# Performance work log

Hardware: AMD Instinct MI355X
Metric: run time of the kernel (lower is better)

The kernel has to match this reference:

```python
import jax, jax.numpy as jnp
import numpy as np

N_NODES = 100000
N_EDGES = 1600000
NUM_RELS = 200
NUM_BASES = 4
IN_FEAT = 20   # hardcoded by `view(-1, 1, 20)` in the torch source
OUT_FEAT = 20
SUBMAT_IN = IN_FEAT // NUM_BASES   # 5
SUBMAT_OUT = OUT_FEAT // NUM_BASES # 5


def setup_inputs() -> dict:
    key = jax.random.key(0)
    ks = jax.random.split(key, 9)
    return {
        "h": jax.random.normal(ks[0], (N_NODES, IN_FEAT), dtype=jnp.float32),
        "weight": jax.random.normal(ks[1], (NUM_RELS, NUM_BASES * SUBMAT_IN * SUBMAT_OUT), dtype=jnp.float32),
        "bias_term": jax.random.normal(ks[2], (NUM_RELS, OUT_FEAT), dtype=jnp.float32),
        "gate_weight": jax.random.normal(ks[3], (NUM_RELS, OUT_FEAT, 1), dtype=jnp.float32),
        "gate_bias": jax.random.normal(ks[4], (NUM_RELS, 1), dtype=jnp.float32),
        "loop_weight": jax.random.normal(ks[5], (IN_FEAT, OUT_FEAT), dtype=jnp.float32),
        "edge_src": jax.random.randint(ks[6], (N_EDGES,), 0, N_NODES, dtype=jnp.int32),
        "edge_dst": jax.random.randint(ks[7], (N_EDGES,), 0, N_NODES, dtype=jnp.int32),
        "etype": jax.random.randint(ks[8], (NUM_RELS,), 0, NUM_RELS, dtype=jnp.int32) if False else jax.random.randint(ks[8], (N_EDGES,), 0, NUM_RELS, dtype=jnp.int32),
    }


def reference(h, weight, bias_term, gate_weight, gate_bias, loop_weight, edge_src, edge_dst, etype):
    n_nodes = h.shape[0]
    # self-loop message (dropout=0.0 -> identity)
    loop_message = h @ loop_weight                                    # [N, out]
    # per-edge relation-indexed gathers
    W = weight[etype].reshape(-1, NUM_BASES, SUBMAT_IN, SUBMAT_OUT)   # [E, B, si, so]
    src = h[edge_src]                                                 # [E, in]
    node = src.reshape(-1, NUM_BASES, SUBMAT_IN)                      # [E, B, si]
    # block-diagonal small matmul
    msg = jnp.einsum('ebi,ebio->ebo', node, W).reshape(-1, OUT_FEAT)  # [E, out]
    # gate: sigmoid(<full src node, gate_weight_r> + gate_bias_r)
    gw = gate_weight[etype, :, 0]                                     # [E, out(=20=in)]
    gb = gate_bias[etype, 0]                                          # [E]
    gate = jax.nn.sigmoid(jnp.sum(src * gw, axis=-1) + gb)            # [E]
    msg = gate[:, None] * (msg + bias_term[etype])                    # [E, out]
    # scatter-sum aggregation to destination nodes (zero init for isolated nodes)
    agg = jax.ops.segment_sum(msg, edge_dst, num_segments=n_nodes)    # [N, out]
    return jax.nn.relu(agg + loop_message)
```

## Files before the change

kernel.cpp:

```cpp
#include <hip/hip_runtime.h>
#include <hip/hip_fp16.h>
#include <math.h>

#define IN_FEAT 20
#define OUT_FEAT 20
#define NUM_BASES 4
#define SUBMAT_IN 5
#define SUBMAT_OUT 5
#define NUM_RELS 200
#define CAP 64
#define NPB 160
#define BCAP 3072
#define EPB 4096


__global__ void __launch_bounds__(256)
hpad_zero_kernel(const float* __restrict__ h, __half* __restrict__ h_pad,
                 int* __restrict__ cursor, int n_nodes, int nb) {
    int v = blockIdx.x * 256 + threadIdx.x;
    if (v < nb) cursor[v] = 0;
    if (v >= n_nodes) return;
    const float4* hp = (const float4*)(h + (size_t)v * IN_FEAT);
    float4 a = hp[0], b = hp[1], c = hp[2], d = hp[3], e = hp[4];
    __half2 p0 = __floats2half2_rn(a.x, a.y), p1 = __floats2half2_rn(a.z, a.w);
    __half2 p2 = __floats2half2_rn(b.x, b.y), p3 = __floats2half2_rn(b.z, b.w);
    __half2 p4 = __floats2half2_rn(c.x, c.y), p5 = __floats2half2_rn(c.z, c.w);
    __half2 p6 = __floats2half2_rn(d.x, d.y), p7 = __floats2half2_rn(d.z, d.w);
    __half2 p8 = __floats2half2_rn(e.x, e.y), p9 = __floats2half2_rn(e.z, e.w);
    uint4 w0, w1; uint2 w2;
    w0.x = *(unsigned*)&p0; w0.y = *(unsigned*)&p1; w0.z = *(unsigned*)&p2; w0.w = *(unsigned*)&p3;
    w1.x = *(unsigned*)&p4; w1.y = *(unsigned*)&p5; w1.z = *(unsigned*)&p6; w1.w = *(unsigned*)&p7;
    w2.x = *(unsigned*)&p8; w2.y = *(unsigned*)&p9;
    char* dst = (char*)(h_pad + (size_t)v * 32);
    *(uint4*)(dst)      = w0;
    *(uint4*)(dst + 16) = w1;
    *(uint2*)(dst + 32) = w2;
}

__global__ void __launch_bounds__(1024)
bucket_scatter_kernel(const int* __restrict__ edge_src,
                      const int* __restrict__ edge_dst,
                      const int* __restrict__ etype,
                      int* __restrict__ cursor,
                      int2* __restrict__ bucketed,
                      int n_edges, int nb) {
    __shared__ int  lhist[640];
    __shared__ int  lofs[640];
    __shared__ int  lrank[640];
    __shared__ int  lbase[640];
    __shared__ int2 img[EPB];
    int tid = threadIdx.x;
    for (int i = tid; i < nb; i += 1024) { lhist[i] = 0; lrank[i] = 0; }
    __syncthreads();

    int blockbase = blockIdx.x * EPB;
    int e0 = blockbase + tid * 4;
    int s[4], d[4], t[4], bk[4];
    bool val[4];
    if (e0 + 3 < n_edges) {
        int4 sv = *(const int4*)(edge_src + e0);
        int4 dv = *(const int4*)(edge_dst + e0);
        int4 tv = *(const int4*)(etype + e0);
        s[0]=sv.x; s[1]=sv.y; s[2]=sv.z; s[3]=sv.w;
        d[0]=dv.x; d[1]=dv.y; d[2]=dv.z; d[3]=dv.w;
        t[0]=tv.x; t[1]=tv.y; t[2]=tv.z; t[3]=tv.w;
        val[0]=val[1]=val[2]=val[3]=true;
    } else {
#pragma unroll
        for (int k = 0; k < 4; ++k) {
            int e = e0 + k;
            val[k] = (e < n_edges);
            s[k] = val[k] ? edge_src[e] : 0;
            d[k] = val[k] ? edge_dst[e] : 0;
            t[k] = val[k] ? etype[e] : 0;
        }
    }
#pragma unroll
    for (int k = 0; k < 4; ++k) {
        bk[k] = d[k] / NPB;
        if (val[k]) atomicAdd(&lhist[bk[k]], 1);
    }
    __syncthreads();

    if (tid < nb) lofs[tid] = lhist[tid];
    __syncthreads();
    for (int step = 1; step < nb; step <<= 1) {
        int v2 = (tid < nb && tid >= step) ? lofs[tid - step] : 0;
        __syncthreads();
        if (tid < nb && tid >= step) lofs[tid] += v2;
        __syncthreads();
    }
    if (tid < nb) {
        lofs[tid] -= lhist[tid];
        if (lhist[tid] > 0) lbase[tid] = atomicAdd(&cursor[tid], lhist[tid]);
    }
    __syncthreads();

#pragma unroll
    for (int k = 0; k < 4; ++k) {
        if (val[k]) {
            int r = atomicAdd(&lrank[bk[k]], 1);
            unsigned packed = (unsigned)s[k] | ((unsigned)t[k] << 17);
            img[lofs[bk[k]] + r] = make_int2(d[k], (int)packed);
        }
    }
    __syncthreads();

    int m = n_edges - blockbase; if (m > EPB) m = EPB;
    for (int i = tid; i < m; i += 1024) {
        int2 e = img[i];
        int b2 = e.x / NPB;
        int dst = lbase[b2] + (i - lofs[b2]);
        if (dst < BCAP) bucketed[(size_t)b2 * BCAP + dst] = e;
    }
}

__global__ void __launch_bounds__(1024)
place_csr_kernel(const int* __restrict__ cursor,
                 const int2* __restrict__ bucketed,
                 unsigned* __restrict__ records,
                 int* __restrict__ cnt,
                 int* __restrict__ off,
                 int n_nodes, int nb) {
    __shared__ int2 simg[BCAP];
    __shared__ int  red[1024];
    __shared__ int  lcnt[NPB];
    __shared__ int  sscan[NPB];
    __shared__ int  lrank[NPB];
    int b = blockIdx.x, tid = threadIdx.x;
    int node0 = b * NPB;

    red[tid] = (tid < b && tid < nb) ? min(cursor[tid], BCAP) : 0;
    if (tid < NPB) { lcnt[tid] = 0; lrank[tid] = 0; }
    __syncthreads();
    for (int step = 512; step > 0; step >>= 1) {
        if (tid < step) red[tid] += red[tid + step];
        __syncthreads();
    }
    int gbase = red[0];

    int m = cursor[b]; if (m > BCAP) m = BCAP;

    for (int i = tid; i < m; i += 1024) {
        int2 r = bucketed[(size_t)b * BCAP + i];
        simg[i] = r;
        atomicAdd(&lcnt[r.x - node0], 1);
    }
    __syncthreads();
    if (tid < NPB) sscan[tid] = lcnt[tid];
    __syncthreads();
    for (int step = 1; step < NPB; step <<= 1) {
        int t = (tid < NPB && tid >= step) ? sscan[tid - step] : 0;
        __syncthreads();
        if (tid < NPB && tid >= step) sscan[tid] += t;
        __syncthreads();
    }
    if (tid < NPB) {
        int excl = sscan[tid] - lcnt[tid];
        int v = node0 + tid;
        if (v < n_nodes) { cnt[v] = lcnt[tid]; off[v] = gbase + excl; }
        sscan[tid] = excl;
    }
    __syncthreads();
    for (int i = tid; i < m; i += 1024) {
        int2 r = simg[i];
        int dl = r.x - node0;
        int rk = atomicAdd(&lrank[dl], 1);
        records[(size_t)gbase + sscan[dl] + rk] = (unsigned)r.y;
    }
}

__global__ void __launch_bounds__(1024, 4)
gather_kernel(const float* __restrict__ h,
              const __half* __restrict__ h_pad,
              const float* __restrict__ loop_weight,
              const float* __restrict__ weight,
              const float* __restrict__ bias_term,
              const float* __restrict__ gate_weight,
              const float* __restrict__ gate_bias,
              const int* __restrict__ cnt,
              const int* __restrict__ off,
              const unsigned* __restrict__ records,
              float* __restrict__ out, int n_nodes, int n_groups) {
    __shared__ __half2 lds_wp[NUM_RELS * 51];
    __shared__ float   lds_gwt[IN_FEAT * NUM_RELS];
    __shared__ float   lds_gb[NUM_RELS];
    __shared__ float   lds_lw[IN_FEAT * OUT_FEAT];
    int tid = threadIdx.x;
    for (int idx = tid; idx < NUM_RELS * 50; idx += 1024) {
        int t = idx / 50, f = idx - t * 50;
        lds_wp[t * 51 + f] = __floats2half2_rn(weight[t * 100 + f],
                                               weight[t * 100 + f + 50]);
    }
    for (int idx = tid; idx < IN_FEAT * NUM_RELS; idx += 1024) {
        int t = idx / IN_FEAT, i = idx - t * IN_FEAT;
        lds_gwt[i * NUM_RELS + t] = gate_weight[idx];
    }
    for (int idx = tid; idx < NUM_RELS; idx += 1024) lds_gb[idx] = gate_bias[idx];
    for (int idx = tid; idx < IN_FEAT * OUT_FEAT; idx += 1024) lds_lw[idx] = loop_weight[idx];
    __syncthreads();

    int wave = blockIdx.x * 16 + (tid >> 6);
    int nwaves = gridDim.x * 16;
    int l = tid & 63;
    int l16 = l & 15;

    for (int grp = wave; grp < n_groups; grp += nwaves) {
        int v = grp * 4 + (l >> 4);
        bool valid = (v < n_nodes);
        int c = 0, base = 0;
        if (valid) { c = cnt[v]; base = off[v]; }
        if (c > CAP) c = CAP;

        float acc[OUT_FEAT];
#pragma unroll
        for (int j = 0; j < OUT_FEAT; ++j) acc[j] = 0.0f;

        if (valid) {
#pragma unroll
            for (int i0 = 0; i0 < 2; ++i0) {
                int i = l16 + i0 * 16;
                if (i < IN_FEAT) {
                    float s = h[(size_t)v * IN_FEAT + i];
#pragma unroll
                    for (int j = 0; j < OUT_FEAT; ++j)
                        acc[j] = fmaf(s, lds_lw[i * OUT_FEAT + j], acc[j]);
                }
            }
        }

#pragma unroll
        for (int it = 0; it < 4; ++it) {
            int slot = l16 + it * 16;
            if (valid && slot < c) {
                unsigned p = records[(size_t)base + slot];
                int srcid = (int)(p & 0x1FFFFu);
                int t = (int)(p >> 17);

                const char* sp = (const char*)(h_pad + (size_t)srcid * 32);
                uint4 A = *(const uint4*)(sp);
                uint4 B = *(const uint4*)(sp + 16);
                uint2 C = *(const uint2*)(sp + 32);
                float src[IN_FEAT];
                {
                    unsigned u[10] = {A.x, A.y, A.z, A.w, B.x, B.y, B.z, B.w, C.x, C.y};
#pragma unroll
                    for (int q = 0; q < 10; ++q) {
                        __half2 hv = *reinterpret_cast<__half2*>(&u[q]);
                        float2 f = __half22float2(hv);
                        src[2 * q] = f.x; src[2 * q + 1] = f.y;
                    }
                }

                float g = lds_gb[t];
#pragma unroll
                for (int i = 0; i < IN_FEAT; ++i)
                    g = fmaf(src[i], lds_gwt[i * NUM_RELS + t], g);
                g = 1.0f / (1.0f + __expf(-g));

#pragma unroll
                for (int i = 0; i < IN_FEAT; ++i) src[i] *= g;

                const __half2* wp = lds_wp + t * 51;
#pragma unroll
                for (int f = 0; f < 50; ++f) {
                    float2 w = __half22float2(wp[f]);
                    const int b0 = f / 25, r = f - b0 * 25;
                    const int i0 = r / 5, o0 = r - i0 * 5;
                    acc[b0 * 5 + o0] =
                        fmaf(src[b0 * 5 + i0], w.x, acc[b0 * 5 + o0]);
                    acc[(b0 + 2) * 5 + o0] =
                        fmaf(src[(b0 + 2) * 5 + i0], w.y, acc[(b0 + 2) * 5 + o0]);
                }

                const float4* btp = (const float4*)(bias_term + (size_t)t * OUT_FEAT);
#pragma unroll
                for (int k = 0; k < OUT_FEAT / 4; ++k) {
                    float4 bv = btp[k];
                    acc[4 * k + 0] = fmaf(g, bv.x, acc[4 * k + 0]);
                    acc[4 * k + 1] = fmaf(g, bv.y, acc[4 * k + 1]);
                    acc[4 * k + 2] = fmaf(g, bv.z, acc[4 * k + 2]);
                    acc[4 * k + 3] = fmaf(g, bv.w, acc[4 * k + 3]);
                }
            }
        }

#pragma unroll
        for (int mask = 8; mask > 0; mask >>= 1) {
#pragma unroll
            for (int j = 0; j < OUT_FEAT; ++j)
                acc[j] += __shfl_xor(acc[j], mask, 16);
        }

        if (valid && l16 < OUT_FEAT / 4) {
            float4 tv;
            tv.x = fmaxf(acc[4 * l16 + 0], 0.0f);
            tv.y = fmaxf(acc[4 * l16 + 1], 0.0f);
            tv.z = fmaxf(acc[4 * l16 + 2], 0.0f);
            tv.w = fmaxf(acc[4 * l16 + 3], 0.0f);
            ((float4*)(out + (size_t)v * OUT_FEAT))[l16] = tv;
        }
    }
}

__global__ void loop_msg_kernel(const float* __restrict__ h,
                                const float* __restrict__ loop_weight,
                                float* __restrict__ out, int n_nodes) {
    int v = blockIdx.x * blockDim.x + threadIdx.x;
    if (v >= n_nodes) return;
    float src[IN_FEAT];
    const float4* hp = (const float4*)(h + (size_t)v * IN_FEAT);
#pragma unroll
    for (int i = 0; i < IN_FEAT / 4; ++i) {
        float4 t = hp[i];
        src[4 * i + 0] = t.x; src[4 * i + 1] = t.y;
        src[4 * i + 2] = t.z; src[4 * i + 3] = t.w;
    }
    float acc[OUT_FEAT];
#pragma unroll
    for (int j = 0; j < OUT_FEAT; ++j) acc[j] = 0.0f;
#pragma unroll
    for (int i = 0; i < IN_FEAT; ++i) {
        float s = src[i];
#pragma unroll
        for (int j = 0; j < OUT_FEAT; ++j)
            acc[j] = fmaf(s, loop_weight[i * OUT_FEAT + j], acc[j]);
    }
    float4* op = (float4*)(out + (size_t)v * OUT_FEAT);
#pragma unroll
    for (int j = 0; j < OUT_FEAT / 4; ++j) {
        float4 t;
        t.x = acc[4 * j + 0]; t.y = acc[4 * j + 1];
        t.z = acc[4 * j + 2]; t.w = acc[4 * j + 3];
        op[j] = t;
    }
}

__global__ void edge_atomic_kernel(const float* __restrict__ h,
                                   const float* __restrict__ weight,
                                   const float* __restrict__ bias_term,
                                   const float* __restrict__ gate_weight,
                                   const float* __restrict__ gate_bias,
                                   const int* __restrict__ edge_src,
                                   const int* __restrict__ edge_dst,
                                   const int* __restrict__ etype,
                                   float* __restrict__ out, int n_edges) {
    int e = blockIdx.x * blockDim.x + threadIdx.x;
    if (e >= n_edges) return;
    int s = edge_src[e], d = edge_dst[e], t = etype[e];
    float src[IN_FEAT];
    const float4* hp = (const float4*)(h + (size_t)s * IN_FEAT);
#pragma unroll
    for (int i = 0; i < IN_FEAT / 4; ++i) {
        float4 v = hp[i];
        src[4 * i + 0] = v.x; src[4 * i + 1] = v.y;
        src[4 * i + 2] = v.z; src[4 * i + 3] = v.w;
    }
    const float* W = weight + (size_t)t * 100;
    float msg[OUT_FEAT];
#pragma unroll
    for (int j = 0; j < OUT_FEAT; ++j) msg[j] = 0.0f;
#pragma unroll
    for (int b = 0; b < NUM_BASES; ++b)
#pragma unroll
        for (int i = 0; i < SUBMAT_IN; ++i) {
            float sv = src[b * SUBMAT_IN + i];
#pragma unroll
            for (int o = 0; o < SUBMAT_OUT; ++o)
                msg[b * SUBMAT_OUT + o] =
                    fmaf(sv, W[(b * SUBMAT_IN + i) * SUBMAT_OUT + o],
                         msg[b * SUBMAT_OUT + o]);
        }
    const float* gw = gate_weight + (size_t)t * OUT_FEAT;
    float g = gate_bias[t];
#pragma unroll
    for (int i = 0; i < IN_FEAT; ++i) g = fmaf(src[i], gw[i], g);
    g = 1.0f / (1.0f + __expf(-g));
    const float* bt = bias_term + (size_t)t * OUT_FEAT;
    float* dstp = out + (size_t)d * OUT_FEAT;
#pragma unroll
    for (int j = 0; j < OUT_FEAT; ++j) atomicAdd(&dstp[j], g * (msg[j] + bt[j]));
}

__global__ void relu_kernel(float* __restrict__ out, int n4) {
    int i = blockIdx.x * blockDim.x + threadIdx.x;
    if (i >= n4) return;
    float4* p = (float4*)out;
    float4 v = p[i];
    v.x = fmaxf(v.x, 0.0f); v.y = fmaxf(v.y, 0.0f);
    v.z = fmaxf(v.z, 0.0f); v.w = fmaxf(v.w, 0.0f);
    p[i] = v;
}

extern "C" void kernel_launch(void* const* d_in, const int* in_sizes, int n_in,
                              void* d_out, int out_size, void* d_ws, size_t ws_size,
                              hipStream_t stream) {
    const float* h           = (const float*)d_in[0];
    const float* weight      = (const float*)d_in[1];
    const float* bias_term   = (const float*)d_in[2];
    const float* gate_weight = (const float*)d_in[3];
    const float* gate_bias   = (const float*)d_in[4];
    const float* loop_weight = (const float*)d_in[5];
    const int* edge_src      = (const int*)d_in[6];
    const int* edge_dst      = (const int*)d_in[7];
    const int* etype         = (const int*)d_in[8];
    float* out = (float*)d_out;

    const int n_nodes = in_sizes[0] / IN_FEAT;
    const int n_edges = in_sizes[6];
    const int nb = (n_nodes + NPB - 1) / NPB;

    size_t off_cursor   = 0;
    size_t off_bucketed = (((size_t)nb * 4 + 127) / 128) * 128;
    size_t off_records  = ((off_bucketed + (size_t)nb * BCAP * 8 + 127) / 128) * 128;
    size_t off_cnt      = ((off_records + (size_t)n_edges * 4 + 127) / 128) * 128;
    size_t off_offs     = ((off_cnt + (size_t)n_nodes * 4 + 127) / 128) * 128;
    size_t off_hpad     = ((off_offs + (size_t)n_nodes * 4 + 127) / 128) * 128;
    size_t need = off_hpad + (size_t)n_nodes * 64;

    bool ok = (ws_size >= need) && (n_nodes <= (1 << 17)) && (nb <= 1024) &&
              (in_sizes[4] == NUM_RELS) && (in_sizes[1] == NUM_RELS * 100) &&
              (in_sizes[5] == IN_FEAT * OUT_FEAT);

    if (ok) {
        int*  cursor      = (int*)((char*)d_ws + off_cursor);
        int2* bucketed    = (int2*)((char*)d_ws + off_bucketed);
        unsigned* records = (unsigned*)((char*)d_ws + off_records);
        int*  cnt         = (int*)((char*)d_ws + off_cnt);
        int*  off         = (int*)((char*)d_ws + off_offs);
        __half* h_pad     = (__half*)((char*)d_ws + off_hpad);

        hpad_zero_kernel<<<(n_nodes + 255) / 256, 256, 0, stream>>>(
            h, h_pad, cursor, n_nodes, nb);
        bucket_scatter_kernel<<<(n_edges + EPB - 1) / EPB, 1024, 0, stream>>>(
            edge_src, edge_dst, etype, cursor, bucketed, n_edges, nb);
        place_csr_kernel<<<nb, 1024, 0, stream>>>(
            cursor, bucketed, records, cnt, off, n_nodes, nb);
        int n_groups = (n_nodes + 3) / 4;
        gather_kernel<<<512, 1024, 0, stream>>>(
            h, h_pad, loop_weight, weight, bias_term, gate_weight, gate_bias,
            cnt, off, records, out, n_nodes, n_groups);
    } else {
        loop_msg_kernel<<<(n_nodes + 255) / 256, 256, 0, stream>>>(
            h, loop_weight, out, n_nodes);
        edge_atomic_kernel<<<(n_edges + 255) / 256, 256, 0, stream>>>(
            h, weight, bias_term, gate_weight, gate_bias,
            edge_src, edge_dst, etype, out, n_edges);
        relu_kernel<<<(n_nodes * OUT_FEAT / 4 + 255) / 256, 256, 0, stream>>>(
            out, n_nodes * OUT_FEAT / 4);
    }
}
```

Measured before the change: 198.7 us.

## Merge h-pad conversion into bucket scatter kernel and use wave-shuffle scans

Folds the fp16 h_pad conversion into the bucket-scatter launch as extra blocks, and zeroes the cursor array with hipMemsetAsync instead. The shared-memory Hillis-Steele scans and the tree reduction, each needing many __syncthreads, are replaced with wavefront shuffle scans followed by a small cross-wave combine. The goal is to cut barrier count and launch overhead in the preprocessing stages. The memset is still a separate stream operation, and the conversion blocks now run at 1024 threads with the larger shared-memory footprint of the scatter kernel.

```diff
diff --git a/kernel.cpp b/kernel.cpp
--- a/kernel.cpp
+++ b/kernel.cpp
@@ -14,42 +14,43 @@
 #define EPB 4096
 
 
-__global__ void __launch_bounds__(256)
-hpad_zero_kernel(const float* __restrict__ h, __half* __restrict__ h_pad,
-                 int* __restrict__ cursor, int n_nodes, int nb) {
-    int v = blockIdx.x * 256 + threadIdx.x;
-    if (v < nb) cursor[v] = 0;
-    if (v >= n_nodes) return;
-    const float4* hp = (const float4*)(h + (size_t)v * IN_FEAT);
-    float4 a = hp[0], b = hp[1], c = hp[2], d = hp[3], e = hp[4];
-    __half2 p0 = __floats2half2_rn(a.x, a.y), p1 = __floats2half2_rn(a.z, a.w);
-    __half2 p2 = __floats2half2_rn(b.x, b.y), p3 = __floats2half2_rn(b.z, b.w);
-    __half2 p4 = __floats2half2_rn(c.x, c.y), p5 = __floats2half2_rn(c.z, c.w);
-    __half2 p6 = __floats2half2_rn(d.x, d.y), p7 = __floats2half2_rn(d.z, d.w);
-    __half2 p8 = __floats2half2_rn(e.x, e.y), p9 = __floats2half2_rn(e.z, e.w);
-    uint4 w0, w1; uint2 w2;
-    w0.x = *(unsigned*)&p0; w0.y = *(unsigned*)&p1; w0.z = *(unsigned*)&p2; w0.w = *(unsigned*)&p3;
-    w1.x = *(unsigned*)&p4; w1.y = *(unsigned*)&p5; w1.z = *(unsigned*)&p6; w1.w = *(unsigned*)&p7;
-    w2.x = *(unsigned*)&p8; w2.y = *(unsigned*)&p9;
-    char* dst = (char*)(h_pad + (size_t)v * 32);
-    *(uint4*)(dst)      = w0;
-    *(uint4*)(dst + 16) = w1;
-    *(uint2*)(dst + 32) = w2;
-}
-
 __global__ void __launch_bounds__(1024)
-bucket_scatter_kernel(const int* __restrict__ edge_src,
-                      const int* __restrict__ edge_dst,
-                      const int* __restrict__ etype,
-                      int* __restrict__ cursor,
-                      int2* __restrict__ bucketed,
-                      int n_edges, int nb) {
+prep_kernel(const float* __restrict__ h, __half* __restrict__ h_pad,
+            const int* __restrict__ edge_src,
+            const int* __restrict__ edge_dst,
+            const int* __restrict__ etype,
+            int* __restrict__ cursor,
+            int2* __restrict__ bucketed,
+            int n_nodes, int n_edges, int nb, int nsb) {
     __shared__ int  lhist[640];
     __shared__ int  lofs[640];
     __shared__ int  lrank[640];
     __shared__ int  lbase[640];
+    __shared__ int  lws[16];
     __shared__ int2 img[EPB];
     int tid = threadIdx.x;
+
+    if (blockIdx.x >= nsb) {
+        int v = (blockIdx.x - nsb) * 1024 + tid;
+        if (v >= n_nodes) return;
+        const float4* hp = (const float4*)(h + (size_t)v * IN_FEAT);
+        float4 a = hp[0], b = hp[1], c = hp[2], d = hp[3], e = hp[4];
+        __half2 p0 = __floats2half2_rn(a.x, a.y), p1 = __floats2half2_rn(a.z, a.w);
+        __half2 p2 = __floats2half2_rn(b.x, b.y), p3 = __floats2half2_rn(b.z, b.w);
+        __half2 p4 = __floats2half2_rn(c.x, c.y), p5 = __floats2half2_rn(c.z, c.w);
+        __half2 p6 = __floats2half2_rn(d.x, d.y), p7 = __floats2half2_rn(d.z, d.w);
+        __half2 p8 = __floats2half2_rn(e.x, e.y), p9 = __floats2half2_rn(e.z, e.w);
+        uint4 w0, w1; uint2 w2;
+        w0.x = *(unsigned*)&p0; w0.y = *(unsigned*)&p1; w0.z = *(unsigned*)&p2; w0.w = *(unsigned*)&p3;
+        w1.x = *(unsigned*)&p4; w1.y = *(unsigned*)&p5; w1.z = *(unsigned*)&p6; w1.w = *(unsigned*)&p7;
+        w2.x = *(unsigned*)&p8; w2.y = *(unsigned*)&p9;
+        char* dst = (char*)(h_pad + (size_t)v * 32);
+        *(uint4*)(dst)      = w0;
+        *(uint4*)(dst + 16) = w1;
+        *(uint2*)(dst + 32) = w2;
+        return;
+    }
+
     for (int i = tid; i < nb; i += 1024) { lhist[i] = 0; lrank[i] = 0; }
     __syncthreads();
 
@@ -82,17 +83,29 @@
     }
     __syncthreads();
 
-    if (tid < nb) lofs[tid] = lhist[tid];
-    __syncthreads();
-    for (int step = 1; step < nb; step <<= 1) {
-        int v2 = (tid < nb && tid >= step) ? lofs[tid - step] : 0;
-        __syncthreads();
-        if (tid < nb && tid >= step) lofs[tid] += v2;
-        __syncthreads();
-    }
+    int hv = (tid < nb) ? lhist[tid] : 0;
+    int x = hv;
+#pragma unroll
+    for (int s2 = 1; s2 < 64; s2 <<= 1) {
+        int y = __shfl_up(x, s2, 64);
+        if ((tid & 63) >= s2) x += y;
+    }
+    if ((tid & 63) == 63) lws[tid >> 6] = x;
+    __syncthreads();
+    if (tid < 16) {
+        int w = lws[tid];
+#pragma unroll
+        for (int s2 = 1; s2 < 16; s2 <<= 1) {
+            int y = __shfl_up(w, s2, 16);
+            if (tid >= s2) w += y;
+        }
+        lws[tid] = w;
+    }
+    __syncthreads();
+    int wb = (tid >> 6) ? lws[(tid >> 6) - 1] : 0;
     if (tid < nb) {
-        lofs[tid] -= lhist[tid];
-        if (lhist[tid] > 0) lbase[tid] = atomicAdd(&cursor[tid], lhist[tid]);
+        lofs[tid] = wb + x - hv;
+        if (hv > 0) lbase[tid] = atomicAdd(&cursor[tid], hv);
     }
     __syncthreads();
 
@@ -123,21 +136,28 @@
                  int* __restrict__ off,
                  int n_nodes, int nb) {
     __shared__ int2 simg[BCAP];
-    __shared__ int  red[1024];
+    __shared__ int  rws[16];
+    __shared__ int  pws[4];
     __shared__ int  lcnt[NPB];
     __shared__ int  sscan[NPB];
     __shared__ int  lrank[NPB];
     int b = blockIdx.x, tid = threadIdx.x;
     int node0 = b * NPB;
 
-    red[tid] = (tid < b && tid < nb) ? min(cursor[tid], BCAP) : 0;
+    int rv = (tid < b && tid < nb) ? min(cursor[tid], BCAP) : 0;
+#pragma unroll
+    for (int s2 = 32; s2 > 0; s2 >>= 1) rv += __shfl_xor(rv, s2, 64);
+    if ((tid & 63) == 0) rws[tid >> 6] = rv;
     if (tid < NPB) { lcnt[tid] = 0; lrank[tid] = 0; }
     __syncthreads();
-    for (int step = 512; step > 0; step >>= 1) {
-        if (tid < step) red[tid] += red[tid + step];
-        __syncthreads();
-    }
-    int gbase = red[0];
+    if (tid == 0) {
+        int s = 0;
+#pragma unroll
+        for (int k = 0; k < 16; ++k) s += rws[k];
+        rws[0] = s;
+    }
+    __syncthreads();
+    int gbase = rws[0];
 
     int m = cursor[b]; if (m > BCAP) m = BCAP;
 
@@ -147,21 +167,35 @@
         atomicAdd(&lcnt[r.x - node0], 1);
     }
     __syncthreads();
-    if (tid < NPB) sscan[tid] = lcnt[tid];
-    __syncthreads();
-    for (int step = 1; step < NPB; step <<= 1) {
-        int t = (tid < NPB && tid >= step) ? sscan[tid - step] : 0;
-        __syncthreads();
-        if (tid < NPB && tid >= step) sscan[tid] += t;
-        __syncthreads();
-    }
+
+    int cv = (tid < NPB) ? lcnt[tid] : 0;
+    int x = cv;
+#pragma unroll
+    for (int s2 = 1; s2 < 64; s2 <<= 1) {
+        int y = __shfl_up(x, s2, 64);
+        if ((tid & 63) >= s2) x += y;
+    }
+    if ((tid & 63) == 63 && (tid >> 6) < 3) pws[tid >> 6] = x;
+    __syncthreads();
+    if (tid < 4) {
+        int w = (tid < 3) ? pws[tid] : 0;
+#pragma unroll
+        for (int s2 = 1; s2 < 4; s2 <<= 1) {
+            int y = __shfl_up(w, s2, 4);
+            if (tid >= s2) w += y;
+        }
+        pws[tid] = w;
+    }
+    __syncthreads();
     if (tid < NPB) {
-        int excl = sscan[tid] - lcnt[tid];
+        int wb = (tid >> 6) ? pws[(tid >> 6) - 1] : 0;
+        int excl = wb + x - cv;
         int v = node0 + tid;
-        if (v < n_nodes) { cnt[v] = lcnt[tid]; off[v] = gbase + excl; }
+        if (v < n_nodes) { cnt[v] = cv; off[v] = gbase + excl; }
         sscan[tid] = excl;
     }
     __syncthreads();
+
     for (int i = tid; i < m; i += 1024) {
         int2 r = simg[i];
         int dl = r.x - node0;
@@ -409,6 +443,8 @@
     const int n_nodes = in_sizes[0] / IN_FEAT;
     const int n_edges = in_sizes[6];
     const int nb = (n_nodes + NPB - 1) / NPB;
+    const int nsb = (n_edges + EPB - 1) / EPB;
+    const int hb = (n_nodes + 1023) / 1024;
 
     size_t off_cursor   = 0;
     size_t off_bucketed = (((size_t)nb * 4 + 127) / 128) * 128;
@@ -430,10 +466,10 @@
         int*  off         = (int*)((char*)d_ws + off_offs);
         __half* h_pad     = (__half*)((char*)d_ws + off_hpad);
 
-        hpad_zero_kernel<<<(n_nodes + 255) / 256, 256, 0, stream>>>(
-            h, h_pad, cursor, n_nodes, nb);
-        bucket_scatter_kernel<<<(n_edges + EPB - 1) / EPB, 1024, 0, stream>>>(
-            edge_src, edge_dst, etype, cursor, bucketed, n_edges, nb);
+        hipMemsetAsync(cursor, 0, (size_t)nb * sizeof(int), stream);
+        prep_kernel<<<nsb + hb, 1024, 0, stream>>>(
+            h, h_pad, edge_src, edge_dst, etype, cursor, bucketed,
+            n_nodes, n_edges, nb, nsb);
         place_csr_kernel<<<nb, 1024, 0, stream>>>(
             cursor, bucketed, records, cnt, off, n_nodes, nb);
         int n_groups = (n_nodes + 3) / 4;
```

Measured after the change: 199.9 us. Within noise of the previous version (+0.6%).
